# Optimization experiments

Hardware: AMD Instinct MI355X
Metric: run time of the kernel (lower is better)

## Reference

```python
import jax, jax.numpy as jnp
import numpy as np

N = 100000
E = 3200000
K = 4
BN_EPS = 1e-5


def spmm(edge_rows, edge_cols, edge_vals, x):
    # y = A @ x with A in COO: y[r] += v * x[c]
    msgs = edge_vals[:, None] * x[edge_cols]           # [E, d]
    return jax.ops.segment_sum(msgs, edge_rows, num_segments=N)


def setup_inputs() -> dict:
    key = jax.random.key(0)
    ks = jax.random.split(key, 8)
    d_in, d_h, d_out = 256, 256, 64
    return {
        "x": jax.random.normal(ks[0], (N, d_in), jnp.float32),
        "edge_rows": jax.random.randint(ks[1], (E,), 0, N, jnp.int32),
        "edge_cols": jax.random.randint(ks[2], (E,), 0, N, jnp.int32),
        "edge_vals": jax.random.uniform(ks[3], (E,), jnp.float32),
        "bn_gamma": jnp.ones((d_in,), jnp.float32),
        "bn_beta": jnp.zeros((d_in,), jnp.float32),
        "w_in": jax.random.normal(ks[4], (d_in, d_h), jnp.float32) * 0.05,
        "b_in": jnp.zeros((d_h,), jnp.float32),
        "w_conv": jax.random.normal(ks[5], (d_h, d_h), jnp.float32) * 0.05,
        "b_conv": jnp.zeros((d_h,), jnp.float32),
        "w_out": jax.random.normal(ks[6], (d_h, d_out), jnp.float32) * 0.05,
        "b_out": jnp.zeros((d_out,), jnp.float32),
    }


def reference(x, edge_rows, edge_cols, edge_vals, bn_gamma, bn_beta,
              w_in, b_in, w_conv, b_conv, w_out, b_out):
    # BatchNorm1d over node dimension (training-mode batch stats, biased var)
    mean = jnp.mean(x, axis=0)
    var = jnp.var(x, axis=0)
    x = (x - mean) * jax.lax.rsqrt(var + BN_EPS) * bn_gamma + bn_beta
    # in_conv + tanh
    x = jnp.tanh(x @ w_in + b_in)
    # SGConv: k spmm hops then linear, then tanh
    for _ in range(K):
        x = spmm(edge_rows, edge_cols, edge_vals, x)
    x = jnp.tanh(x @ w_conv + b_conv)
    # out_conv (logits)
    return x @ w_out + b_out
```

## Files before the change

### kernel.cpp

```cpp
#include <hip/hip_runtime.h>
#include <hip/hip_fp16.h>

#define NN   100000
#define NNP  100096
#define EE   3200000
#define DD   256
#define DOUTC 64
#define LSTR 40

#define NBK  782
#define PB   512
#define CHUNK 6250
#define STATB 512

typedef _Float16 half8 __attribute__((ext_vector_type(8)));
typedef _Float16 half4 __attribute__((ext_vector_type(4)));
typedef float    f32x4 __attribute__((ext_vector_type(4)));

__device__ inline f32x4 mfma16(half8 a, half8 b, f32x4 c) {
    return __builtin_amdgcn_mfma_f32_16x16x32_f16(a, b, c, 0, 0, 0);
}

__global__ __launch_bounds__(256) void col_stats_kernel(
        const float* __restrict__ x, float* __restrict__ stats) {
    __shared__ float4 shs[4][64];
    __shared__ float4 shs2[4][64];
    int tid = threadIdx.x;
    int c4 = tid & 63;
    int rq = tid >> 6;
    float4 s  = make_float4(0.f, 0.f, 0.f, 0.f);
    float4 s2 = make_float4(0.f, 0.f, 0.f, 0.f);
    for (int r = blockIdx.x * 4 + rq; r < NN; r += STATB * 4) {
        float4 v = *(const float4*)&x[(size_t)r * DD + c4 * 4];
        s.x += v.x; s.y += v.y; s.z += v.z; s.w += v.w;
        s2.x += v.x * v.x; s2.y += v.y * v.y; s2.z += v.z * v.z; s2.w += v.w * v.w;
    }
    shs[rq][c4] = s;
    shs2[rq][c4] = s2;
    __syncthreads();
    if (rq == 0) {
#pragma unroll
        for (int q = 1; q < 4; ++q) {
            float4 a = shs[q][c4], b = shs2[q][c4];
            s.x += a.x; s.y += a.y; s.z += a.z; s.w += a.w;
            s2.x += b.x; s2.y += b.y; s2.z += b.z; s2.w += b.w;
        }
        atomicAdd(&stats[c4 * 4 + 0], s.x);
        atomicAdd(&stats[c4 * 4 + 1], s.y);
        atomicAdd(&stats[c4 * 4 + 2], s.z);
        atomicAdd(&stats[c4 * 4 + 3], s.w);
        atomicAdd(&stats[DD + c4 * 4 + 0], s2.x);
        atomicAdd(&stats[DD + c4 * 4 + 1], s2.y);
        atomicAdd(&stats[DD + c4 * 4 + 2], s2.z);
        atomicAdd(&stats[DD + c4 * 4 + 3], s2.w);
    }
}

__global__ void fold_bias_kernel(const float* __restrict__ stats,
                                 const float* __restrict__ gamma,
                                 const float* __restrict__ beta,
                                 const float* __restrict__ w_in,
                                 const float* __restrict__ b_in,
                                 float* __restrict__ bfold) {
    __shared__ float sb[DD];
    int t = threadIdx.x;
    float mean = stats[t] * (1.0f / NN);
    float var  = stats[DD + t] * (1.0f / NN) - mean * mean;
    float a = gamma[t] * rsqrtf(var + 1e-5f);
    sb[t] = beta[t] - mean * a;
    __syncthreads();
    float acc = 0.f;
    for (int j = 0; j < DD; ++j) acc += sb[j] * w_in[j * DD + t];
    bfold[t] = b_in[t] + acc;
}

__global__ void split_w1_kernel(const float* __restrict__ stats,
                                const float* __restrict__ gamma,
                                const float* __restrict__ w_in,
                                _Float16* __restrict__ wth, _Float16* __restrict__ wtl) {
    int k = blockIdx.x, n = threadIdx.x;
    float mean = stats[k] * (1.0f / NN);
    float var  = stats[DD + k] * (1.0f / NN) - mean * mean;
    float a = gamma[k] * rsqrtf(var + 1e-5f);
    float v = a * w_in[(size_t)k * DD + n];
    _Float16 hi = (_Float16)v;
    _Float16 lo = (_Float16)(v - (float)hi);
    wth[(size_t)n * DD + k] = hi;
    wtl[(size_t)n * DD + k] = lo;
}

__global__ void split_w_kernel(const float* __restrict__ w, int ncols,
                               _Float16* __restrict__ wth, _Float16* __restrict__ wtl) {
    int k = blockIdx.x, n = threadIdx.x;
    float v = w[(size_t)k * ncols + n];
    _Float16 hi = (_Float16)v;
    _Float16 lo = (_Float16)(v - (float)hi);
    wth[(size_t)n * DD + k] = hi;
    wtl[(size_t)n * DD + k] = lo;
}

__global__ __launch_bounds__(256) void bucket_count_kernel(
        const int* __restrict__ rows, int* __restrict__ Cm) {
    __shared__ int bins[NBK];
    int t = threadIdx.x;
    for (int i = t; i < NBK; i += 256) bins[i] = 0;
    __syncthreads();
    int base = blockIdx.x * CHUNK;
    for (int e = base + t; e < base + CHUNK; e += 256) {
        int r = __builtin_nontemporal_load(&rows[e]);
        atomicAdd(&bins[r >> 7], 1);
    }
    __syncthreads();
    for (int i = t; i < NBK; i += 256) Cm[(size_t)blockIdx.x * NBK + i] = bins[i];
}

__global__ __launch_bounds__(256) void scan_col_kernel(int* __restrict__ Cm,
                                                       int* __restrict__ Tb) {
    __shared__ int s[256];
    int b = blockIdx.x;
    int t = threadIdx.x;
    int v0 = Cm[(size_t)(2 * t)     * NBK + b];
    int v1 = Cm[(size_t)(2 * t + 1) * NBK + b];
    int local = v0 + v1;
    s[t] = local;
    __syncthreads();
    for (int off = 1; off < 256; off <<= 1) {
        int xv = 0;
        if (t >= off) xv = s[t - off];
        __syncthreads();
        if (t >= off) s[t] += xv;
        __syncthreads();
    }
    int excl = s[t] - local;
    Cm[(size_t)(2 * t)     * NBK + b] = excl;
    Cm[(size_t)(2 * t + 1) * NBK + b] = excl + v0;
    if (t == 255) Tb[b] = s[255];
}

__global__ __launch_bounds__(256) void scan_buckets_kernel(const int* __restrict__ Tb,
                                                           int* __restrict__ Bb) {
    __shared__ int s[256];
    int t = threadIdx.x;
    int v[4]; int local = 0;
    for (int i = 0; i < 4; ++i) {
        int idx = t * 4 + i;
        v[i] = (idx < NBK) ? Tb[idx] : 0;
        local += v[i];
    }
    s[t] = local;
    __syncthreads();
    for (int off = 1; off < 256; off <<= 1) {
        int xv = 0;
        if (t >= off) xv = s[t - off];
        __syncthreads();
        if (t >= off) s[t] += xv;
        __syncthreads();
    }
    int excl = s[t] - local;
    int run = excl;
    for (int i = 0; i < 4; ++i) {
        int idx = t * 4 + i;
        if (idx < NBK) Bb[idx] = run;
        run += v[i];
    }
    if (t == 255) Bb[NBK] = EE;
}

__global__ __launch_bounds__(256) void bucket_scatter_kernel(
        const int* __restrict__ rows, const int* __restrict__ cols,
        const float* __restrict__ vals, const int* __restrict__ Cm,
        const int* __restrict__ Bb, int2* __restrict__ ebuf) {
    __shared__ int bins[NBK];
    int t = threadIdx.x;
    for (int i = t; i < NBK; i += 256) bins[i] = 0;
    __syncthreads();
    int base = blockIdx.x * CHUNK;
    for (int e = base + t; e < base + CHUNK; e += 256) {
        int r = __builtin_nontemporal_load(&rows[e]);
        int c = __builtin_nontemporal_load(&cols[e]);
        float v = __builtin_nontemporal_load(&vals[e]);
        int bkt = r >> 7;
        int lr = atomicAdd(&bins[bkt], 1);
        int pos = Bb[bkt] + Cm[(size_t)blockIdx.x * NBK + bkt] + lr;
        ebuf[pos] = make_int2(c | ((r & 127) << 17), __float_as_int(v));
    }
}

__global__ __launch_bounds__(256) void bucket_finalize_kernel(
        const int* __restrict__ Bb, const int2* __restrict__ ebuf,
        int* __restrict__ rp, int2* __restrict__ edges) {
    __shared__ int hist[128];
    __shared__ int excl[128];
    __shared__ int cur[128];
    __shared__ int sc[128];
    int b = blockIdx.x;
    int t = threadIdx.x;
    int e0 = Bb[b], e1 = Bb[b + 1];
    if (t < 128) { hist[t] = 0; cur[t] = 0; }
    __syncthreads();
    for (int e = e0 + t; e < e1; e += 256)
        atomicAdd(&hist[ebuf[e].x >> 17], 1);
    __syncthreads();
    if (t < 128) sc[t] = hist[t];
    __syncthreads();
    for (int off = 1; off < 128; off <<= 1) {
        int xv = 0;
        if (t < 128 && t >= off) xv = sc[t - off];
        __syncthreads();
        if (t < 128 && t >= off) sc[t] += xv;
        __syncthreads();
    }
    if (t < 128) {
        excl[t] = sc[t] - hist[t];
        int gr = b * 128 + t;
        if (gr < NN) rp[gr] = e0 + excl[t];
    }
    if (b == 0 && t == 0) rp[NN] = EE;
    __syncthreads();
    for (int e = e0 + t; e < e1; e += 256) {
        int2 d = ebuf[e];
        int rl = d.x >> 17;
        int lr = atomicAdd(&cur[rl], 1);
        edges[e0 + excl[rl] + lr] = make_int2(d.x & 0x1FFFF, d.y);
    }
}

__global__ __launch_bounds__(256) void spmm_kernel(
        const int* __restrict__ rp, const int2* __restrict__ edges,
        const __half* __restrict__ xin, __half* __restrict__ xout, int ph) {
    int tid = threadIdx.x;
    int lane = tid & 63;
    int sub = lane >> 4;
    int sl = lane & 15;
    int r = __builtin_amdgcn_readfirstlane(blockIdx.x * 4 + (tid >> 6));
    int e0 = rp[r], e1 = rp[r + 1];
    const float4* xi = (const float4*)xin;
    const long long* epk = (const long long*)edges;
    int cbase = ph * 16 + sl;

    float acc[8] = {0.f,0.f,0.f,0.f,0.f,0.f,0.f,0.f};

    int base = e0;
    for (; base + 8 <= e1; base += 8) {
        long long p0 = __builtin_nontemporal_load(&epk[base + sub]);
        long long p1 = __builtin_nontemporal_load(&epk[base + 4 + sub]);
        int c0 = (int)(unsigned int)p0, c1 = (int)(unsigned int)p1;
        float v0 = __int_as_float((int)(p0 >> 32));
        float v1 = __int_as_float((int)(p1 >> 32));
        float4 x0 = xi[(size_t)c0 * 32 + cbase];
        float4 x1 = xi[(size_t)c1 * 32 + cbase];
        {
            const __half2* hp = (const __half2*)&x0;
            float2 f0 = __half22float2(hp[0]);
            float2 f1 = __half22float2(hp[1]);
            float2 f2 = __half22float2(hp[2]);
            float2 f3 = __half22float2(hp[3]);
            acc[0] += v0*f0.x; acc[1] += v0*f0.y;
            acc[2] += v0*f1.x; acc[3] += v0*f1.y;
            acc[4] += v0*f2.x; acc[5] += v0*f2.y;
            acc[6] += v0*f3.x; acc[7] += v0*f3.y;
        }
        {
            const __half2* hp = (const __half2*)&x1;
            float2 f0 = __half22float2(hp[0]);
            float2 f1 = __half22float2(hp[1]);
            float2 f2 = __half22float2(hp[2]);
            float2 f3 = __half22float2(hp[3]);
            acc[0] += v1*f0.x; acc[1] += v1*f0.y;
            acc[2] += v1*f1.x; acc[3] += v1*f1.y;
            acc[4] += v1*f2.x; acc[5] += v1*f2.y;
            acc[6] += v1*f3.x; acc[7] += v1*f3.y;
        }
    }
    if (base < e1) {
#pragma unroll
        for (int i = 0; i < 2; ++i) {
            int idx = base + 4*i + sub;
            bool valid = idx < e1;
            int idxc = valid ? idx : e0;
            long long p = epk[idxc];
            int c = (int)(unsigned int)p;
            float v = valid ? __int_as_float((int)(p >> 32)) : 0.f;
            float4 xv = xi[(size_t)c * 32 + cbase];
            const __half2* hp = (const __half2*)&xv;
            float2 f0 = __half22float2(hp[0]);
            float2 f1 = __half22float2(hp[1]);
            float2 f2 = __half22float2(hp[2]);
            float2 f3 = __half22float2(hp[3]);
            acc[0] += v*f0.x; acc[1] += v*f0.y;
            acc[2] += v*f1.x; acc[3] += v*f1.y;
            acc[4] += v*f2.x; acc[5] += v*f2.y;
            acc[6] += v*f3.x; acc[7] += v*f3.y;
        }
    }
#pragma unroll
    for (int j = 0; j < 8; ++j) {
        acc[j] += __shfl_xor(acc[j], 16, 64);
        acc[j] += __shfl_xor(acc[j], 32, 64);
    }
    if (sub == 0) {
        union { __half h[8]; f32x4 f; } u;
#pragma unroll
        for (int j = 0; j < 8; ++j) u.h[j] = __float2half_rn(acc[j]);
        __builtin_nontemporal_store(u.f, (f32x4*)&((float4*)xout)[(size_t)r * 32 + cbase]);
    }
}

template<bool SPLIT_A, bool TANH, typename Tout, int BN>
__global__ __launch_bounds__(256) void gemm_mfma(
    const void* __restrict__ Av, const _Float16* __restrict__ WTh,
    const _Float16* __restrict__ WTl, const float* __restrict__ bias,
    Tout* __restrict__ C, int M_A, int M_C, int NC)
{
    __shared__ _Float16 As_hi[128 * LSTR];
    __shared__ _Float16 As_lo[(SPLIT_A ? 128 : 1) * LSTR];
    __shared__ _Float16 Ws_hi[BN * LSTR];
    __shared__ _Float16 Ws_lo[BN * LSTR];

    int tid = threadIdx.x;
    int lane = tid & 63;
    int w = tid >> 6;
    int q = lane >> 4;
    int r16 = lane & 15;
    int m0 = blockIdx.x * 128;
    int n0 = blockIdx.y * BN;

    constexpr int MT = (BN == 128) ? 4 : 2;
    int wm = (BN == 128) ? (w & 1) * 64 : w * 32;
    int wn = (BN == 128) ? (w >> 1) * 64 : 0;

    f32x4 acc[MT][4];
#pragma unroll
    for (int mt = 0; mt < MT; ++mt)
#pragma unroll
        for (int nt = 0; nt < 4; ++nt) acc[mt][nt] = (f32x4){0.f, 0.f, 0.f, 0.f};

    for (int k0 = 0; k0 < 256; k0 += 32) {
        if (SPLIT_A) {
            const float* A = (const float*)Av;
#pragma unroll
            for (int p = 0; p < 4; ++p) {
                int idx = tid + p * 256;
                int m = idx >> 3, kc = idx & 7;
                int gm = m0 + m;
                float4 av = make_float4(0.f, 0.f, 0.f, 0.f);
                if (gm < M_A) av = *(const float4*)&A[(size_t)gm * 256 + k0 + kc * 4];
                half4 hi, lo;
                hi.x = (_Float16)av.x; lo.x = (_Float16)(av.x - (float)hi.x);
                hi.y = (_Float16)av.y; lo.y = (_Float16)(av.y - (float)hi.y);
                hi.z = (_Float16)av.z; lo.z = (_Float16)(av.z - (float)hi.z);
                hi.w = (_Float16)av.w; lo.w = (_Float16)(av.w - (float)hi.w);
                *(half4*)&As_hi[m * LSTR + kc * 4] = hi;
                *(half4*)&As_lo[m * LSTR + kc * 4] = lo;
            }
        } else {
            const _Float16* A = (const _Float16*)Av;
#pragma unroll
            for (int p = 0; p < 2; ++p) {
                int idx = tid + p * 256;
                int m = idx >> 2, kc = idx & 3;
                half8 av = *(const half8*)&A[(size_t)(m0 + m) * 256 + k0 + kc * 8];
                *(half8*)&As_hi[m * LSTR + kc * 8] = av;
            }
        }
#pragma unroll
        for (int p = 0; p < BN / 64; ++p) {
            int idx = tid + p * 256;
            int n = idx >> 2, kc = idx & 3;
            *(half8*)&Ws_hi[n * LSTR + kc * 8] = *(const half8*)&WTh[(size_t)(n0 + n) * 256 + k0 + kc * 8];
            *(half8*)&Ws_lo[n * LSTR + kc * 8] = *(const half8*)&WTl[(size_t)(n0 + n) * 256 + k0 + kc * 8];
        }
        __syncthreads();

        half8 af_h[MT], af_l[MT], wf_h[4], wf_l[4];
#pragma unroll
        for (int mt = 0; mt < MT; ++mt) {
            int mrow = wm + mt * 16 + r16;
            af_h[mt] = *(const half8*)&As_hi[mrow * LSTR + q * 8];
            if (SPLIT_A) af_l[mt] = *(const half8*)&As_lo[mrow * LSTR + q * 8];
        }
#pragma unroll
        for (int nt = 0; nt < 4; ++nt) {
            int nrow = wn + nt * 16 + r16;
            wf_h[nt] = *(const half8*)&Ws_hi[nrow * LSTR + q * 8];
            wf_l[nt] = *(const half8*)&Ws_lo[nrow * LSTR + q * 8];
        }
#pragma unroll
        for (int mt = 0; mt < MT; ++mt)
#pragma unroll
            for (int nt = 0; nt < 4; ++nt) {
                acc[mt][nt] = mfma16(af_h[mt], wf_h[nt], acc[mt][nt]);
                if (SPLIT_A) acc[mt][nt] = mfma16(af_l[mt], wf_h[nt], acc[mt][nt]);
                acc[mt][nt] = mfma16(af_h[mt], wf_l[nt], acc[mt][nt]);
            }
        __syncthreads();
    }

#pragma unroll
    for (int nt = 0; nt < 4; ++nt) {
        float b = bias[n0 + wn + nt * 16 + r16];
        int gc = n0 + wn + nt * 16 + r16;
#pragma unroll
        for (int mt = 0; mt < MT; ++mt) {
#pragma unroll
            for (int r = 0; r < 4; ++r) {
                int gm = m0 + wm + mt * 16 + q * 4 + r;
                float v = acc[mt][nt][r] + b;
                if (TANH) v = tanhf(v);
                if (gm < M_C) C[(size_t)gm * NC + gc] = (Tout)v;
            }
        }
    }
}

extern "C" void kernel_launch(void* const* d_in, const int* in_sizes, int n_in,
                              void* d_out, int out_size, void* d_ws, size_t ws_size,
                              hipStream_t stream) {
    const float* x      = (const float*)d_in[0];
    const int*   erows  = (const int*)d_in[1];
    const int*   ecols  = (const int*)d_in[2];
    const float* evals  = (const float*)d_in[3];
    const float* gamma  = (const float*)d_in[4];
    const float* beta   = (const float*)d_in[5];
    const float* w_in   = (const float*)d_in[6];
    const float* b_in   = (const float*)d_in[7];
    const float* w_conv = (const float*)d_in[8];
    const float* b_conv = (const float*)d_in[9];
    const float* w_out  = (const float*)d_in[10];
    const float* b_out  = (const float*)d_in[11];
    float* out = (float*)d_out;

    char* ws = (char*)d_ws;
    size_t off = 0;
    auto alloc = [&](size_t bytes) -> void* {
        void* p = ws + off;
        off = (off + bytes + 255) & ~(size_t)255;
        return p;
    };
    _Float16* h1   = (_Float16*)alloc((size_t)NNP * DD * 2);
    _Float16* h2   = (_Float16*)alloc((size_t)NNP * DD * 2);
    int2*  edges = (int2*) alloc((size_t)EE * 8);
    int2*  ebuf  = (int2*) alloc((size_t)EE * 8);
    int*   Cm    = (int*)  alloc((size_t)PB * NBK * 4);
    int*   Tb    = (int*)  alloc((size_t)NBK * 4);
    int*   Bb    = (int*)  alloc((size_t)(NBK + 1) * 4);
    int*   rp    = (int*)  alloc((size_t)(NN + 1) * 4);
    float* stats = (float*)alloc(2 * DD * 4);
    _Float16* wt1h = (_Float16*)alloc((size_t)DD * DD * 2);
    _Float16* wt1l = (_Float16*)alloc((size_t)DD * DD * 2);
    _Float16* wt2h = (_Float16*)alloc((size_t)DD * DD * 2);
    _Float16* wt2l = (_Float16*)alloc((size_t)DD * DD * 2);
    _Float16* wt3h = (_Float16*)alloc((size_t)DOUTC * DD * 2);
    _Float16* wt3l = (_Float16*)alloc((size_t)DOUTC * DD * 2);
    float* bfold = (float*)alloc(DD * 4);

    hipMemsetAsync(stats, 0, 2 * DD * 4, stream);

    bucket_count_kernel<<<PB, 256, 0, stream>>>(erows, Cm);
    scan_col_kernel<<<NBK, 256, 0, stream>>>(Cm, Tb);
    scan_buckets_kernel<<<1, 256, 0, stream>>>(Tb, Bb);
    bucket_scatter_kernel<<<PB, 256, 0, stream>>>(erows, ecols, evals, Cm, Bb, ebuf);
    bucket_finalize_kernel<<<NBK, 256, 0, stream>>>(Bb, ebuf, rp, edges);

    col_stats_kernel<<<STATB, 256, 0, stream>>>(x, stats);
    fold_bias_kernel<<<1, 256, 0, stream>>>(stats, gamma, beta, w_in, b_in, bfold);
    split_w1_kernel<<<DD, DD, 0, stream>>>(stats, gamma, w_in, wt1h, wt1l);
    split_w_kernel<<<DD, DD, 0, stream>>>(w_conv, DD, wt2h, wt2l);
    split_w_kernel<<<DD, DOUTC, 0, stream>>>(w_out, DOUTC, wt3h, wt3l);

    dim3 g2(NNP / 128, 2), g1(NNP / 128, 1);
    gemm_mfma<true, true, _Float16, 128><<<g2, 256, 0, stream>>>(
        x, wt1h, wt1l, bfold, h1, NN, NNP, DD);

    spmm_kernel<<<NN / 4, 256, 0, stream>>>(rp, edges, (const __half*)h1, (__half*)h2, 0);
    spmm_kernel<<<NN / 4, 256, 0, stream>>>(rp, edges, (const __half*)h1, (__half*)h2, 1);
    spmm_kernel<<<NN / 4, 256, 0, stream>>>(rp, edges, (const __half*)h2, (__half*)h1, 0);
    spmm_kernel<<<NN / 4, 256, 0, stream>>>(rp, edges, (const __half*)h2, (__half*)h1, 1);
    spmm_kernel<<<NN / 4, 256, 0, stream>>>(rp, edges, (const __half*)h1, (__half*)h2, 0);
    spmm_kernel<<<NN / 4, 256, 0, stream>>>(rp, edges, (const __half*)h1, (__half*)h2, 1);
    spmm_kernel<<<NN / 4, 256, 0, stream>>>(rp, edges, (const __half*)h2, (__half*)h1, 0);
    spmm_kernel<<<NN / 4, 256, 0, stream>>>(rp, edges, (const __half*)h2, (__half*)h1, 1);

    gemm_mfma<false, true, _Float16, 128><<<g2, 256, 0, stream>>>(
        h1, wt2h, wt2l, b_conv, h2, NNP, NNP, DD);
    gemm_mfma<false, false, float, 64><<<g1, 256, 0, stream>>>(
        h2, wt3h, wt3l, b_out, out, NNP, NN, DOUTC);
}
```

Baseline: 1.494 ms.

## Merge SpMM column phases, pre-split input during stats pass, use fast tanh

SpMM now processes all 256 columns per row in one launch, with 32 lanes per edge and 4 edges per lane group in flight. This halves the number of SpMM launches and edge-list reads per hop. The column-stats pass now also writes the fp16 hi/lo split of x, so the first GEMM loads pre-split halves instead of converting fp32 per tile, at the cost of extra workspace and an extra write of x. tanhf is replaced by an exp/rcp approximation, which may slightly change accuracy.

Measured after the change: 1.504 ms. No clear change (+0.6%).

```diff
diff --git a/kernel.cpp b/kernel.cpp
--- a/kernel.cpp
+++ b/kernel.cpp
@@ -21,8 +21,15 @@
     return __builtin_amdgcn_mfma_f32_16x16x32_f16(a, b, c, 0, 0, 0);
 }
 
+__device__ inline float fast_tanh(float v) {
+    float e = __expf(2.0f * v);
+    return 1.0f - 2.0f * __builtin_amdgcn_rcpf(e + 1.0f);
+}
+
+template<bool WSPLIT>
 __global__ __launch_bounds__(256) void col_stats_kernel(
-        const float* __restrict__ x, float* __restrict__ stats) {
+        const float* __restrict__ x, float* __restrict__ stats,
+        _Float16* __restrict__ xh, _Float16* __restrict__ xl) {
     __shared__ float4 shs[4][64];
     __shared__ float4 shs2[4][64];
     int tid = threadIdx.x;
@@ -34,6 +41,15 @@
         float4 v = *(const float4*)&x[(size_t)r * DD + c4 * 4];
         s.x += v.x; s.y += v.y; s.z += v.z; s.w += v.w;
         s2.x += v.x * v.x; s2.y += v.y * v.y; s2.z += v.z * v.z; s2.w += v.w * v.w;
+        if (WSPLIT) {
+            half4 hi, lo;
+            hi.x = (_Float16)v.x; lo.x = (_Float16)(v.x - (float)hi.x);
+            hi.y = (_Float16)v.y; lo.y = (_Float16)(v.y - (float)hi.y);
+            hi.z = (_Float16)v.z; lo.z = (_Float16)(v.z - (float)hi.z);
+            hi.w = (_Float16)v.w; lo.w = (_Float16)(v.w - (float)hi.w);
+            *(half4*)&xh[(size_t)r * DD + c4 * 4] = hi;
+            *(half4*)&xl[(size_t)r * DD + c4 * 4] = lo;
+        }
     }
     shs[rq][c4] = s;
     shs2[rq][c4] = s2;
@@ -227,61 +243,54 @@
 
 __global__ __launch_bounds__(256) void spmm_kernel(
         const int* __restrict__ rp, const int2* __restrict__ edges,
-        const __half* __restrict__ xin, __half* __restrict__ xout, int ph) {
+        const __half* __restrict__ xin, __half* __restrict__ xout) {
     int tid = threadIdx.x;
     int lane = tid & 63;
-    int sub = lane >> 4;
-    int sl = lane & 15;
+    int sub = lane >> 5;
+    int sl = lane & 31;
     int r = __builtin_amdgcn_readfirstlane(blockIdx.x * 4 + (tid >> 6));
     int e0 = rp[r], e1 = rp[r + 1];
     const float4* xi = (const float4*)xin;
     const long long* epk = (const long long*)edges;
-    int cbase = ph * 16 + sl;
 
     float acc[8] = {0.f,0.f,0.f,0.f,0.f,0.f,0.f,0.f};
 
     int base = e0;
     for (; base + 8 <= e1; base += 8) {
-        long long p0 = __builtin_nontemporal_load(&epk[base + sub]);
-        long long p1 = __builtin_nontemporal_load(&epk[base + 4 + sub]);
-        int c0 = (int)(unsigned int)p0, c1 = (int)(unsigned int)p1;
-        float v0 = __int_as_float((int)(p0 >> 32));
-        float v1 = __int_as_float((int)(p1 >> 32));
-        float4 x0 = xi[(size_t)c0 * 32 + cbase];
-        float4 x1 = xi[(size_t)c1 * 32 + cbase];
-        {
-            const __half2* hp = (const __half2*)&x0;
+        long long p[4];
+#pragma unroll
+        for (int i = 0; i < 4; ++i)
+            p[i] = __builtin_nontemporal_load(&epk[base + sub * 4 + i]);
+        float4 xv[4];
+#pragma unroll
+        for (int i = 0; i < 4; ++i) {
+            int c = (int)(unsigned int)p[i];
+            xv[i] = xi[(size_t)c * 32 + sl];
+        }
+#pragma unroll
+        for (int i = 0; i < 4; ++i) {
+            float v = __int_as_float((int)(p[i] >> 32));
+            const __half2* hp = (const __half2*)&xv[i];
             float2 f0 = __half22float2(hp[0]);
             float2 f1 = __half22float2(hp[1]);
             float2 f2 = __half22float2(hp[2]);
             float2 f3 = __half22float2(hp[3]);
-            acc[0] += v0*f0.x; acc[1] += v0*f0.y;
-            acc[2] += v0*f1.x; acc[3] += v0*f1.y;
-            acc[4] += v0*f2.x; acc[5] += v0*f2.y;
-            acc[6] += v0*f3.x; acc[7] += v0*f3.y;
-        }
-        {
-            const __half2* hp = (const __half2*)&x1;
-            float2 f0 = __half22float2(hp[0]);
-            float2 f1 = __half22float2(hp[1]);
-            float2 f2 = __half22float2(hp[2]);
-            float2 f3 = __half22float2(hp[3]);
-            acc[0] += v1*f0.x; acc[1] += v1*f0.y;
-            acc[2] += v1*f1.x; acc[3] += v1*f1.y;
-            acc[4] += v1*f2.x; acc[5] += v1*f2.y;
-            acc[6] += v1*f3.x; acc[7] += v1*f3.y;
+            acc[0] += v*f0.x; acc[1] += v*f0.y;
+            acc[2] += v*f1.x; acc[3] += v*f1.y;
+            acc[4] += v*f2.x; acc[5] += v*f2.y;
+            acc[6] += v*f3.x; acc[7] += v*f3.y;
         }
     }
     if (base < e1) {
 #pragma unroll
-        for (int i = 0; i < 2; ++i) {
-            int idx = base + 4*i + sub;
+        for (int i = 0; i < 4; ++i) {
+            int idx = base + 2 * i + sub;
             bool valid = idx < e1;
             int idxc = valid ? idx : e0;
             long long p = epk[idxc];
             int c = (int)(unsigned int)p;
             float v = valid ? __int_as_float((int)(p >> 32)) : 0.f;
-            float4 xv = xi[(size_t)c * 32 + cbase];
+            float4 xv = xi[(size_t)c * 32 + sl];
             const __half2* hp = (const __half2*)&xv;
             float2 f0 = __half22float2(hp[0]);
             float2 f1 = __half22float2(hp[1]);
@@ -294,26 +303,23 @@
         }
     }
 #pragma unroll
-    for (int j = 0; j < 8; ++j) {
-        acc[j] += __shfl_xor(acc[j], 16, 64);
-        acc[j] += __shfl_xor(acc[j], 32, 64);
-    }
+    for (int j = 0; j < 8; ++j) acc[j] += __shfl_xor(acc[j], 32, 64);
     if (sub == 0) {
         union { __half h[8]; f32x4 f; } u;
 #pragma unroll
         for (int j = 0; j < 8; ++j) u.h[j] = __float2half_rn(acc[j]);
-        __builtin_nontemporal_store(u.f, (f32x4*)&((float4*)xout)[(size_t)r * 32 + cbase]);
-    }
-}
-
-template<bool SPLIT_A, bool TANH, typename Tout, int BN>
+        __builtin_nontemporal_store(u.f, (f32x4*)&((float4*)xout)[(size_t)r * 32 + sl]);
+    }
+}
+
+template<int AMODE, bool TANH, typename Tout, int BN>
 __global__ __launch_bounds__(256) void gemm_mfma(
-    const void* __restrict__ Av, const _Float16* __restrict__ WTh,
-    const _Float16* __restrict__ WTl, const float* __restrict__ bias,
-    Tout* __restrict__ C, int M_A, int M_C, int NC)
+    const void* __restrict__ Av, const _Float16* __restrict__ Al,
+    const _Float16* __restrict__ WTh, const _Float16* __restrict__ WTl,
+    const float* __restrict__ bias, Tout* __restrict__ C, int M_A, int M_C, int NC)
 {
     __shared__ _Float16 As_hi[128 * LSTR];
-    __shared__ _Float16 As_lo[(SPLIT_A ? 128 : 1) * LSTR];
+    __shared__ _Float16 As_lo[(AMODE != 1 ? 128 : 1) * LSTR];
     __shared__ _Float16 Ws_hi[BN * LSTR];
     __shared__ _Float16 Ws_lo[BN * LSTR];
 
@@ -336,7 +342,7 @@
         for (int nt = 0; nt < 4; ++nt) acc[mt][nt] = (f32x4){0.f, 0.f, 0.f, 0.f};
 
     for (int k0 = 0; k0 < 256; k0 += 32) {
-        if (SPLIT_A) {
+        if (AMODE == 0) {
             const float* A = (const float*)Av;
 #pragma unroll
             for (int p = 0; p < 4; ++p) {
@@ -359,8 +365,11 @@
             for (int p = 0; p < 2; ++p) {
                 int idx = tid + p * 256;
                 int m = idx >> 2, kc = idx & 3;
-                half8 av = *(const half8*)&A[(size_t)(m0 + m) * 256 + k0 + kc * 8];
-                *(half8*)&As_hi[m * LSTR + kc * 8] = av;
+                *(half8*)&As_hi[m * LSTR + kc * 8] =
+                    *(const half8*)&A[(size_t)(m0 + m) * 256 + k0 + kc * 8];
+                if (AMODE == 2)
+                    *(half8*)&As_lo[m * LSTR + kc * 8] =
+                        *(const half8*)&Al[(size_t)(m0 + m) * 256 + k0 + kc * 8];
             }
         }
 #pragma unroll
@@ -377,7 +386,7 @@
         for (int mt = 0; mt < MT; ++mt) {
             int mrow = wm + mt * 16 + r16;
             af_h[mt] = *(const half8*)&As_hi[mrow * LSTR + q * 8];
-            if (SPLIT_A) af_l[mt] = *(const half8*)&As_lo[mrow * LSTR + q * 8];
+            if (AMODE != 1) af_l[mt] = *(const half8*)&As_lo[mrow * LSTR + q * 8];
         }
 #pragma unroll
         for (int nt = 0; nt < 4; ++nt) {
@@ -390,7 +399,7 @@
 #pragma unroll
             for (int nt = 0; nt < 4; ++nt) {
                 acc[mt][nt] = mfma16(af_h[mt], wf_h[nt], acc[mt][nt]);
-                if (SPLIT_A) acc[mt][nt] = mfma16(af_l[mt], wf_h[nt], acc[mt][nt]);
+                if (AMODE != 1) acc[mt][nt] = mfma16(af_l[mt], wf_h[nt], acc[mt][nt]);
                 acc[mt][nt] = mfma16(af_h[mt], wf_l[nt], acc[mt][nt]);
             }
         __syncthreads();
@@ -406,7 +415,7 @@
             for (int r = 0; r < 4; ++r) {
                 int gm = m0 + wm + mt * 16 + q * 4 + r;
                 float v = acc[mt][nt][r] + b;
-                if (TANH) v = tanhf(v);
+                if (TANH) v = fast_tanh(v);
                 if (gm < M_C) C[(size_t)gm * NC + gc] = (Tout)v;
             }
         }
@@ -453,6 +462,9 @@
     _Float16* wt3h = (_Float16*)alloc((size_t)DOUTC * DD * 2);
     _Float16* wt3l = (_Float16*)alloc((size_t)DOUTC * DD * 2);
     float* bfold = (float*)alloc(DD * 4);
+    _Float16* xh = h2;
+    _Float16* xl = (_Float16*)alloc((size_t)NNP * DD * 2);
+    bool presplit = (off <= ws_size);
 
     hipMemsetAsync(stats, 0, 2 * DD * 4, stream);
 
@@ -462,27 +474,34 @@
     bucket_scatter_kernel<<<PB, 256, 0, stream>>>(erows, ecols, evals, Cm, Bb, ebuf);
     bucket_finalize_kernel<<<NBK, 256, 0, stream>>>(Bb, ebuf, rp, edges);
 
-    col_stats_kernel<<<STATB, 256, 0, stream>>>(x, stats);
+    if (presplit) {
+        hipMemsetAsync(xh + (size_t)NN * DD, 0, (size_t)(NNP - NN) * DD * 2, stream);
+        hipMemsetAsync(xl + (size_t)NN * DD, 0, (size_t)(NNP - NN) * DD * 2, stream);
+        col_stats_kernel<true><<<STATB, 256, 0, stream>>>(x, stats, xh, xl);
+    } else {
+        col_stats_kernel<false><<<STATB, 256, 0, stream>>>(x, stats, nullptr, nullptr);
+    }
     fold_bias_kernel<<<1, 256, 0, stream>>>(stats, gamma, beta, w_in, b_in, bfold);
     split_w1_kernel<<<DD, DD, 0, stream>>>(stats, gamma, w_in, wt1h, wt1l);
     split_w_kernel<<<DD, DD, 0, stream>>>(w_conv, DD, wt2h, wt2l);
     split_w_kernel<<<DD, DOUTC, 0, stream>>>(w_out, DOUTC, wt3h, wt3l);
 
     dim3 g2(NNP / 128, 2), g1(NNP / 128, 1);
-    gemm_mfma<true, true, _Float16, 128><<<g2, 256, 0, stream>>>(
-        x, wt1h, wt1l, bfold, h1, NN, NNP, DD);
-
-    spmm_kernel<<<NN / 4, 256, 0, stream>>>(rp, edges, (const __half*)h1, (__half*)h2, 0);
-    spmm_kernel<<<NN / 4, 256, 0, stream>>>(rp, edges, (const __half*)h1, (__half*)h2, 1);
-    spmm_kernel<<<NN / 4, 256, 0, stream>>>(rp, edges, (const __half*)h2, (__half*)h1, 0);
-    spmm_kernel<<<NN / 4, 256, 0, stream>>>(rp, edges, (const __half*)h2, (__half*)h1, 1);
-    spmm_kernel<<<NN / 4, 256, 0, stream>>>(rp, edges, (const __half*)h1, (__half*)h2, 0);
-    spmm_kernel<<<NN / 4, 256, 0, stream>>>(rp, edges, (const __half*)h1, (__half*)h2, 1);
-    spmm_kernel<<<NN / 4, 256, 0, stream>>>(rp, edges, (const __half*)h2, (__half*)h1, 0);
-    spmm_kernel<<<NN / 4, 256, 0, stream>>>(rp, edges, (const __half*)h2, (__half*)h1, 1);
-
-    gemm_mfma<false, true, _Float16, 128><<<g2, 256, 0, stream>>>(
-        h1, wt2h, wt2l, b_conv, h2, NNP, NNP, DD);
-    gemm_mfma<false, false, float, 64><<<g1, 256, 0, stream>>>(
-        h2, wt3h, wt3l, b_out, out, NNP, NN, DOUTC);
-}
+    if (presplit) {
+        gemm_mfma<2, true, _Float16, 128><<<g2, 256, 0, stream>>>(
+            xh, xl, wt1h, wt1l, bfold, h1, NNP, NNP, DD);
+    } else {
+        gemm_mfma<0, true, _Float16, 128><<<g2, 256, 0, stream>>>(
+            x, nullptr, wt1h, wt1l, bfold, h1, NN, NNP, DD);
+    }
+
+    spmm_kernel<<<NN / 4, 256, 0, stream>>>(rp, edges, (const __half*)h1, (__half*)h2);
+    spmm_kernel<<<NN / 4, 256, 0, stream>>>(rp, edges, (const __half*)h2, (__half*)h1);
+    spmm_kernel<<<NN / 4, 256, 0, stream>>>(rp, edges, (const __half*)h1, (__half*)h2);
+    spmm_kernel<<<NN / 4, 256, 0, stream>>>(rp, edges, (const __half*)h2, (__half*)h1);
+
+    gemm_mfma<1, true, _Float16, 128><<<g2, 256, 0, stream>>>(
+        h1, nullptr, wt2h, wt2l, b_conv, h2, NNP, NNP, DD);
+    gemm_mfma<1, false, float, 64><<<g1, 256, 0, stream>>>(
+        h2, nullptr, wt3h, wt3l, b_out, out, NNP, NN, DOUTC);
+}
```
